# Kernel tuning notes

Hardware: AMD Instinct MI355X
Metric: run time of the kernel (lower is better)

Reference implementation:

```python
import jax, jax.numpy as jnp
import numpy as np

B, C, H, W = 64, 3, 224, 224
PH = PW = 16
GH, GW = H // PH, W // PW
NP = GH * GW                        # 196 patches
E = 512                             # embed_dim == decoder_dim
NH = 8                              # num_heads
PPD = C * PH * PW                   # 768 pixels per patch
MASK_RATIO = 0.75
NUM_MASKED = int(MASK_RATIO * NP)   # 147


def setup_inputs() -> dict:
    key = jax.random.key(0)
    ks = jax.random.split(key, 16)
    s = 0.02
    x = jax.random.normal(ks[0], (B, C, H, W), jnp.float32)
    # per-sample random permutation (torch.rand().argsort() equivalent)
    shuffle_indices = jax.vmap(lambda k: jax.random.permutation(k, NP))(
        jax.random.split(ks[1], B)).astype(jnp.int32)
    return {
        "x": x,
        "shuffle_indices": shuffle_indices,
        "W_pe": jax.random.normal(ks[2], (E, PPD), jnp.float32) * s,
        "b_pe": jnp.zeros((E,), jnp.float32),
        "pos_embed": jax.random.normal(ks[3], (1, NP, E), jnp.float32),
        "enc_W": jax.random.normal(ks[4], (E, E), jnp.float32) * s,
        "enc_b": jnp.zeros((E,), jnp.float32),
        "in_proj_w": jax.random.normal(ks[5], (3 * E, E), jnp.float32) * s,
        "in_proj_b": jnp.zeros((3 * E,), jnp.float32),
        "out_w": jax.random.normal(ks[6], (E, E), jnp.float32) * s,
        "out_b": jnp.zeros((E,), jnp.float32),
        "head_W": jax.random.normal(ks[7], (PPD, E), jnp.float32) * s,
        "head_b": jnp.zeros((PPD,), jnp.float32),
        # torch.randn_like(mask_patches) noise, passed in for determinism
        "noise": jax.random.normal(ks[8], (B, NUM_MASKED, PPD), jnp.float32),
    }


def _to_img(p):
    # [b, nP, ph*pw*c] -> [b, c, H, W] (inverse of patchify)
    return p.reshape(B, GH, GW, PH, PW, C).transpose(0, 5, 1, 3, 2, 4).reshape(B, C, H, W)


def reference(x, shuffle_indices, W_pe, b_pe, pos_embed, enc_W, enc_b,
              in_proj_w, in_proj_b, out_w, out_b, head_W, head_b, noise):
    hd = E // NH
    # patchify: [b,c,H,W] -> [b, nP, ph*pw*c]
    patches = x.reshape(B, C, GH, PH, GW, PW).transpose(0, 2, 4, 3, 5, 1).reshape(B, NP, PPD)

    mask_ind = shuffle_indices[:, :NUM_MASKED]      # [b, 147]
    unmask_ind = shuffle_indices[:, NUM_MASKED:]    # [b, 49]
    bi = jnp.arange(B)[:, None]
    mask_patches = patches[bi, mask_ind]            # [b,147,768]
    unmask_patches = patches[bi, unmask_ind]        # [b, 49,768]

    # mask_image: unmasked patches copied from x, masked patches = 1
    is_masked = jnp.zeros((B, NP), bool).at[bi, mask_ind].set(True)
    mpix = is_masked.reshape(B, 1, GH, 1, GW, 1)
    mpix = jnp.broadcast_to(mpix, (B, C, GH, PH, GW, PW)).reshape(B, C, H, W)
    mask_image = jnp.where(mpix, jnp.ones_like(x), x)

    # encode visible tokens
    pe = pos_embed[0]                               # [nP, E]
    unmask_tokens = unmask_patches @ W_pe.T + b_pe + pe[unmask_ind]
    encoded = jax.nn.gelu(unmask_tokens @ enc_W.T + enc_b)   # encoder.transformer stand-in

    # decode: cross attention (queries = mask tokens, kv = encoded)
    mask_tokens = mask_patches @ W_pe.T + b_pe + pe[mask_ind]
    Wq, Wk, Wv = jnp.split(in_proj_w, 3)
    bq, bk, bv = jnp.split(in_proj_b, 3)
    q = (mask_tokens @ Wq.T + bq).reshape(B, NUM_MASKED, NH, hd)
    k = (encoded @ Wk.T + bk).reshape(B, -1, NH, hd)
    v = (encoded @ Wv.T + bv).reshape(B, -1, NH, hd)
    attn = jax.nn.softmax(jnp.einsum('bqhd,bkhd->bhqk', q, k) / jnp.sqrt(jnp.float32(hd)), axis=-1)
    attn_out = jnp.einsum('bhqk,bkhd->bqhd', attn, v).reshape(B, NUM_MASKED, E) @ out_w.T + out_b

    # scatter encoded + attended tokens back into full sequence
    output_tokens = (jnp.zeros((B, NP, E), x.dtype)
                     .at[bi, unmask_ind].set(encoded)
                     .at[bi, mask_ind].set(attn_out))
    dec_mask_tokens = output_tokens[bi, mask_ind]
    pred = dec_mask_tokens @ head_W.T + head_b      # [b,147,768]

    mse_all_patches = jnp.abs(pred - mask_patches).mean(axis=-1).mean()

    recons_patches = jax.lax.stop_gradient(patches).at[bi, mask_ind].set(pred)
    recons_img = _to_img(recons_patches)

    patches_noisy = patches.at[bi, mask_ind].set(noise)
    patches_to_img = _to_img(patches_noisy)

    return recons_img, patches_to_img, mse_all_patches, mask_image
```

## Files before the change

kernel.cpp:

```cpp
#include <hip/hip_runtime.h>
#include <math.h>

typedef __attribute__((ext_vector_type(8))) __bf16 bf16x8;
typedef __attribute__((ext_vector_type(8))) unsigned short u16x8;
typedef __attribute__((ext_vector_type(4))) unsigned short u16x4;
typedef __attribute__((ext_vector_type(4))) float f32x4;

typedef unsigned int as1_u32 __attribute__((address_space(1)));
typedef unsigned int as3_u32 __attribute__((address_space(3)));

__device__ __forceinline__ float bf2f(unsigned short h){
  return __uint_as_float(((unsigned int)h) << 16);
}
__device__ __forceinline__ unsigned short f2bf(float f){
  unsigned int u = __float_as_uint(f);
  unsigned int r = (u + 0x7FFFu + ((u >> 16) & 1u)) >> 16;
  return (unsigned short)r;
}

#if __has_builtin(__builtin_amdgcn_global_load_lds)
#define HAVE_GLOAD_LDS 1
__device__ __forceinline__ void gload16(const void* g, void* l){
  __builtin_amdgcn_global_load_lds((const as1_u32*)(unsigned long long)g,
                                   (as3_u32*)l, 16, 0, 0);
}
#else
#define HAVE_GLOAD_LDS 0
#endif

__global__ __launch_bounds__(256) void prep_all(
    const int* __restrict__ shuf, int* __restrict__ slot, int* __restrict__ invp,
    const float* __restrict__ Wpe, const float* __restrict__ outw,
    unsigned short* __restrict__ WpeT, unsigned short* __restrict__ outwT,
    const float* __restrict__ encW, const float* __restrict__ inW,
    const float* __restrict__ headW, unsigned short* __restrict__ wcat,
    const float* __restrict__ pos, const float* __restrict__ b_pe,
    const float* __restrict__ outb, const float* __restrict__ headb,
    unsigned short* __restrict__ pe2b, float* __restrict__ bh32)
{
  const int bid = blockIdx.x, t = threadIdx.x;
  __shared__ float tile[32][33];
  if (bid < 49){
    const int i = bid*256 + t;
    if (i < 64*196){
      const int b = i / 196, j = i % 196;
      const int p = shuf[b*196 + j];
      slot[b*196 + p] = (j < 147) ? j : -1;
      invp[b*196 + p] = j;
    }
  } else if (bid < 689){
    int b2 = bid - 49;
    const float* src; unsigned short* dst; int R, C, bx, by;
    if (b2 < 384){ src = Wpe;  dst = WpeT;  R = 512; C = 768; bx = b2 % 24; by = b2 / 24; }
    else { b2 -= 384; src = outw; dst = outwT; R = 512; C = 512; bx = b2 % 16; by = b2 / 16; }
    const int tx = t & 31, ty = t >> 5;
    #pragma unroll
    for (int i = 0; i < 4; i++)
      tile[ty + i*8][tx] = src[(size_t)(by*32 + ty + i*8)*C + bx*32 + tx];
    __syncthreads();
    #pragma unroll
    for (int i = 0; i < 4; i++)
      dst[(size_t)(bx*32 + ty + i*8)*R + by*32 + tx] = f2bf(tile[tx][ty + i*8]);
  } else if (bid < 2097){
    const int i = ((bid - 689)*256 + t) * 4;
    f32x4 v;
    if      (i <  262144) v = *(const f32x4*)(encW + i);
    else if (i < 1048576) v = *(const f32x4*)(inW + (i - 262144));
    else                  v = *(const f32x4*)(headW + (i - 1048576));
    u16x4 o = { f2bf(v[0]), f2bf(v[1]), f2bf(v[2]), f2bf(v[3]) };
    *(u16x4*)(wcat + i) = o;
  } else if (bid < 2225){
    const int i = ((bid - 2097)*256 + t) * 4;
    u16x4 o = {0, 0, 0, 0};
    if (i < 100352){
      const f32x4 pv = *(const f32x4*)(pos + i);
      const f32x4 bv = *(const f32x4*)(b_pe + (i & 511));
      o = u16x4{ f2bf(pv[0]+bv[0]), f2bf(pv[1]+bv[1]), f2bf(pv[2]+bv[2]), f2bf(pv[3]+bv[3]) };
    }
    *(u16x4*)(pe2b + i) = o;
  } else {
    const int r = (bid - 2225)*64 + (t >> 2);
    const int q4 = t & 3;
    float a = 0.0f;
    const float* hw = headW + (size_t)r*512 + q4*128;
    const float* ob = outb + q4*128;
    for (int e = 0; e < 128; e++) a += hw[e] * ob[e];
    a += __shfl_down(a, 2, 4);
    a += __shfl_down(a, 1, 4);
    if (q4 == 0) bh32[r] = a + headb[r];
  }
}

struct GD {
  const unsigned short* A; const unsigned short* W; const float* aux;
  const int* tok; unsigned short* ob; float* of;
  int N, K, mode, blk0, nx;
};

__device__ __forceinline__ void gemm_core(const GD g, int local, unsigned char* smem){
  const int tn = (local % g.nx) * 64;
  const int tm = (local / g.nx) * 128;
  const int N = g.N, K = g.K;
  unsigned short* As = (unsigned short*)smem;
  unsigned short* Bs = (unsigned short*)(smem + 2*128*32*2);
  const int t = threadIdx.x;
  const int wave = t >> 6, lane = t & 63;
  const int wr = (wave >> 1) * 64, wc = (wave & 1) * 32;
  const int lr = lane & 15, lg = lane >> 4;

  f32x4 acc[4][2] = {};
  const int nt = K >> 5;

#if HAVE_GLOAD_LDS
  const int srow = lane >> 2;
  const int scol = (lane & 3) * 8;
  const unsigned short* Ag = g.A + (size_t)(tm + wave*32 + srow) * K + scol;
  const unsigned short* Bg = g.W + (size_t)(tn + wave*16 + srow) * K + scol;
  const size_t rstepA = (size_t)16 * K;

  auto issue = [&](int tile_i, int slot_i){
    const int k0 = tile_i * 32;
    unsigned short* Al = As + slot_i*(128*32) + wave*(32*32);
    unsigned short* Bl = Bs + slot_i*(64*32)  + wave*(16*32);
    gload16(Ag + k0,          Al);
    gload16(Ag + k0 + rstepA, Al + 16*32);
    gload16(Bg + k0,          Bl);
  };

  issue(0, 0);
  __syncthreads();

  for (int tt = 0; tt < nt; ++tt){
    const int cur = tt & 1;
    if (tt + 1 < nt) issue(tt + 1, cur ^ 1);
    const unsigned short* Ab = As + cur*(128*32);
    const unsigned short* Bb = Bs + cur*(64*32);
    bf16x8 av[4], bv[2];
    #pragma unroll
    for (int mi = 0; mi < 4; mi++) av[mi] = *(const bf16x8*)&Ab[(wr + mi*16 + lr)*32 + lg*8];
    #pragma unroll
    for (int ni = 0; ni < 2; ni++) bv[ni] = *(const bf16x8*)&Bb[(wc + ni*16 + lr)*32 + lg*8];
    #pragma unroll
    for (int mi = 0; mi < 4; mi++)
      #pragma unroll
      for (int ni = 0; ni < 2; ni++)
        acc[mi][ni] = __builtin_amdgcn_mfma_f32_16x16x32_bf16(av[mi], bv[ni], acc[mi][ni], 0, 0, 0);
    __syncthreads();
  }
#else
  unsigned short* As1 = (unsigned short*)smem;
  unsigned short* Bs1 = (unsigned short*)(smem + 128*32*2);
  const int r0 = t >> 2;
  const int c0 = (t & 3) * 8;
  for (int k0 = 0; k0 < K; k0 += 32){
    u16x8 ra0 = *(const u16x8*)(g.A + (size_t)(tm + r0) * K + k0 + c0);
    u16x8 rb0 = (r0 < 64) ? *(const u16x8*)(g.W + (size_t)(tn + r0) * K + k0 + c0) : u16x8{};
    __syncthreads();
    *(u16x8*)&As1[r0 * 32 + c0] = ra0;
    if (r0 < 64) *(u16x8*)&Bs1[r0 * 32 + c0] = rb0;
    __syncthreads();
    bf16x8 av[4], bv[2];
    #pragma unroll
    for (int mi = 0; mi < 4; mi++) av[mi] = *(const bf16x8*)&As1[(wr + mi*16 + lr)*32 + lg*8];
    #pragma unroll
    for (int ni = 0; ni < 2; ni++) bv[ni] = *(const bf16x8*)&Bs1[(wc + ni*16 + lr)*32 + lg*8];
    #pragma unroll
    for (int mi = 0; mi < 4; mi++)
      #pragma unroll
      for (int ni = 0; ni < 2; ni++)
        acc[mi][ni] = __builtin_amdgcn_mfma_f32_16x16x32_bf16(av[mi], bv[ni], acc[mi][ni], 0, 0, 0);
  }
#endif

  const int mode = g.mode;
  #pragma unroll
  for (int ni = 0; ni < 2; ni++){
    const int gcol = tn + wc + ni*16 + lr;
    const float bval = (mode == 0 || mode == 3) ? g.aux[gcol] : 0.0f;
    #pragma unroll
    for (int mi = 0; mi < 4; mi++){
      #pragma unroll
      for (int jj = 0; jj < 4; jj++){
        const int grow = tm + wr + mi*16 + lg*4 + jj;
        float v = acc[mi][ni][jj] + bval;
        if (mode == 1 || mode == 2) v += g.aux[(size_t)(g.tok[grow] & 255) * 512 + gcol];
        if (mode == 2){
          const float u = v;
          v = 0.5f * u * (1.0f + tanhf(0.7978845608f * (u + 0.044715f * u * u * u)));
        }
        if (mode == 3) g.of[(size_t)grow * N + gcol] = v;
        else           g.ob[(size_t)grow * N + gcol] = f2bf(v);
      }
    }
  }
}

__global__ __launch_bounds__(256) void gemm_one(GD g){
  __shared__ __align__(16) unsigned char smem[24576];
  gemm_core(g, blockIdx.x, smem);
}
__global__ __launch_bounds__(256) void gemm_two(GD a, GD b){
  __shared__ __align__(16) unsigned char smem[24576];
  GD g = (blockIdx.x >= b.blk0) ? b : a;
  gemm_core(g, blockIdx.x - g.blk0, smem);
}

__global__ __launch_bounds__(256) void fold_patch(GD g0, GD g1, GD g2, GD g3, GD g4,
    const float* __restrict__ x, const int* __restrict__ invp,
    unsigned short* __restrict__ maskA, unsigned short* __restrict__ unmaskA,
    int* __restrict__ tokcat)
{
  __shared__ __align__(16) unsigned char smem[24576];
  const int bid = blockIdx.x, t = threadIdx.x;
  if (bid < 176){
    GD g = g0;
    if (bid >= g1.blk0) g = g1;
    if (bid >= g2.blk0) g = g2;
    if (bid >= g3.blk0) g = g3;
    if (bid >= g4.blk0) g = g4;
    gemm_core(g, bid - g.blk0, smem);
    return;
  }
  const int blk = bid - 176;
  const int b = blk / 14, gh = blk % 14;
  unsigned short* ld = (unsigned short*)smem;
  for (int e = t; e < 2688; e += 256){
    const int w4 = e % 56, rest = e / 56;
    const int phi = rest & 15, c = rest >> 4;
    const f32x4 v4 = *(const f32x4*)(x + (size_t)b*150528 + c*50176
                                     + (size_t)(gh*16 + phi)*224 + w4*4);
    const int gw = w4 >> 2, part = w4 & 3;
    const int dbase = gw*768 + phi*48 + part*12 + c;
    ld[dbase]     = f2bf(v4[0]);
    ld[dbase + 3] = f2bf(v4[1]);
    ld[dbase + 6] = f2bf(v4[2]);
    ld[dbase + 9] = f2bf(v4[3]);
  }
  __syncthreads();
  for (int e = t; e < 1344; e += 256){
    const int gw = e / 96, elem8 = e % 96;
    const int p = gh*14 + gw;
    const int j = invp[b*196 + p];
    unsigned short* dst;
    int row;
    if (j < 147){ row = b*160 + j;        dst = maskA; }
    else        { row = b*64 + (j - 147); dst = unmaskA; }
    *(u16x8*)&dst[(size_t)row*768 + elem8*8] = *(const u16x8*)&ld[gw*768 + elem8*8];
    if (elem8 == 0) tokcat[(j < 147) ? (b*160 + j) : (10240 + b*64 + (j - 147))] = p;
  }
}

__global__ __launch_bounds__(256) void attn_mfma(const unsigned short* __restrict__ qb,
                                                 const unsigned short* __restrict__ kv,
                                                 unsigned short* __restrict__ attnout)
{
  __shared__ __align__(16) unsigned char smem[72064];
  unsigned short* qs  = (unsigned short*)smem;
  unsigned short* ks  = (unsigned short*)(smem + 27648);
  unsigned short* vsT = (unsigned short*)(smem + 36864);
  unsigned short* pwt = (unsigned short*)(smem + 46080);
  float* inv_ = (float*)(smem + 71424);
  const int b = blockIdx.x >> 3, h = blockIdx.x & 7;
  const int t = threadIdx.x;
  const int wave = t >> 6, lane = t & 63;
  const int wr = (wave >> 1) * 96, wc = (wave & 1) * 32;
  const int lr = lane & 15, lg = lane >> 4;

  for (int idx = t; idx < 192*8; idx += 256){
    const int i = idx >> 3, g = idx & 7;
    u16x8 v = {};
    if (i < 160) v = *(const u16x8*)(qb + (size_t)(b*160 + i)*512 + h*64 + g*8);
    *(u16x8*)&qs[i*72 + g*8] = v;
  }
  for (int idx = t; idx < 64*8; idx += 256){
    const int j = idx >> 3, g = idx & 7;
    const size_t base = (size_t)(b*64 + j)*1024 + h*64 + g*8;
    u16x8 k8 = *(const u16x8*)(kv + base);
    u16x8 v8 = *(const u16x8*)(kv + base + 512);
    *(u16x8*)&ks[j*72 + g*8] = k8;
    #pragma unroll
    for (int d = 0; d < 8; d++) vsT[(g*8 + d)*72 + j] = v8[d];
  }
  __syncthreads();

  {
    f32x4 acc[6][2] = {};
    #pragma unroll
    for (int ksv = 0; ksv < 2; ksv++){
      const int kk = ksv*32;
      bf16x8 av[6], bv[2];
      #pragma unroll
      for (int mi = 0; mi < 6; mi++) av[mi] = *(const bf16x8*)&qs[(wr + mi*16 + lr)*72 + kk + lg*8];
      #pragma unroll
      for (int ni = 0; ni < 2; ni++) bv[ni] = *(const bf16x8*)&ks[(wc + ni*16 + lr)*72 + kk + lg*8];
      #pragma unroll
      for (int mi = 0; mi < 6; mi++)
        #pragma unroll
        for (int ni = 0; ni < 2; ni++)
          acc[mi][ni] = __builtin_amdgcn_mfma_f32_16x16x32_bf16(av[mi], bv[ni], acc[mi][ni], 0, 0, 0);
    }
    #pragma unroll
    for (int mi = 0; mi < 6; mi++)
      #pragma unroll
      for (int ni = 0; ni < 2; ni++)
        #pragma unroll
        for (int jj = 0; jj < 4; jj++)
          pwt[(wr + mi*16 + lg*4 + jj)*66 + wc + ni*16 + lr] = f2bf(acc[mi][ni][jj] * 0.125f);
  }
  __syncthreads();

  unsigned short* pa = qs;
  if (t < 147){
    float sc[49];
    float m = -1e30f;
    #pragma unroll 7
    for (int j = 0; j < 49; j++){ sc[j] = bf2f(pwt[t*66 + j]); m = fmaxf(m, sc[j]); }
    float sum = 0.0f;
    for (int j = 0; j < 49; j++){
      const float e = __expf(sc[j] - m);
      sum += e;
      pa[t*72 + j] = f2bf(e);
    }
    inv_[t] = 1.0f / sum;
    for (int j = 49; j < 64; j++) pa[t*72 + j] = 0;
  } else if (t < 192){
    for (int j = 0; j < 64; j++) pa[t*72 + j] = 0;
    if (t < 160) inv_[t] = 0.0f;
  }
  __syncthreads();

  {
    f32x4 acc[6][2] = {};
    #pragma unroll
    for (int ksv = 0; ksv < 2; ksv++){
      const int kk = ksv*32;
      bf16x8 av[6], bv[2];
      #pragma unroll
      for (int mi = 0; mi < 6; mi++) av[mi] = *(const bf16x8*)&pa[(wr + mi*16 + lr)*72 + kk + lg*8];
      #pragma unroll
      for (int ni = 0; ni < 2; ni++) bv[ni] = *(const bf16x8*)&vsT[(wc + ni*16 + lr)*72 + kk + lg*8];
      #pragma unroll
      for (int mi = 0; mi < 6; mi++)
        #pragma unroll
        for (int ni = 0; ni < 2; ni++)
          acc[mi][ni] = __builtin_amdgcn_mfma_f32_16x16x32_bf16(av[mi], bv[ni], acc[mi][ni], 0, 0, 0);
    }
    #pragma unroll
    for (int mi = 0; mi < 6; mi++)
      #pragma unroll
      for (int ni = 0; ni < 2; ni++)
        #pragma unroll
        for (int jj = 0; jj < 4; jj++){
          const int grow = wr + mi*16 + lg*4 + jj;
          if (grow < 160){
            const float v = acc[mi][ni][jj] * inv_[grow];
            attnout[(size_t)(b*160 + grow)*512 + h*64 + wc + ni*16 + lr] = f2bf(v);
          }
        }
  }
}

__global__ __launch_bounds__(256) void finalize_k(const float* __restrict__ x, const int* __restrict__ slot,
                           const unsigned short* __restrict__ predb, const float* __restrict__ noise,
                           float* __restrict__ out, float* __restrict__ partial)
{
  const int i4 = blockIdx.x * 256 + threadIdx.x;
  const int idx = i4 * 4;
  const int w = idx % 224;
  const int h = (idx / 224) % 224;
  const int c = (idx / 50176) % 3;
  const int b = idx / 150528;
  const f32x4 xv = *(const f32x4*)(x + idx);
  const int p = (h >> 4) * 14 + (w >> 4);
  const int s = slot[b*196 + p];
  f32x4 rec = xv, noi = xv, mim = xv;
  float a = 0.0f;
  if (s >= 0){
    const int d = (h & 15)*48 + (w & 15)*3 + c;
    const size_t pb = (size_t)(b*160 + s)*768 + d;
    const size_t nb = (size_t)(b*147 + s)*768 + d;
    rec = f32x4{bf2f(predb[pb]), bf2f(predb[pb+3]), bf2f(predb[pb+6]), bf2f(predb[pb+9])};
    noi = f32x4{noise[nb], noise[nb+3], noise[nb+6], noise[nb+9]};
    mim = f32x4{1.0f, 1.0f, 1.0f, 1.0f};
    a = fabsf(rec[0] - xv[0]) + fabsf(rec[1] - xv[1]) + fabsf(rec[2] - xv[2]) + fabsf(rec[3] - xv[3]);
  }
  *(f32x4*)(out + idx) = rec;
  *(f32x4*)(out + 9633792 + idx) = noi;
  float prevm = __shfl_up(mim[3], 1);
  if ((threadIdx.x & 63) == 0 && idx > 0){
    const int pidx = idx - 1;
    const int pw2 = pidx % 224, ph2 = (pidx / 224) % 224;
    const int pb2 = pidx / 150528;
    const int pp = (ph2 >> 4) * 14 + (pw2 >> 4);
    prevm = (slot[pb2*196 + pp] >= 0) ? 1.0f : x[pidx];
  }
  *(f32x4*)(out + 19267584 + idx) = f32x4{prevm, mim[0], mim[1], mim[2]};
  if (i4 == 2408447) out[28901376] = mim[3];
  #pragma unroll
  for (int o = 32; o > 0; o >>= 1) a += __shfl_down(a, o);
  __shared__ float wsum[4];
  if ((threadIdx.x & 63) == 0) wsum[threadIdx.x >> 6] = a;
  __syncthreads();
  if (threadIdx.x == 0)
    partial[blockIdx.x] = wsum[0] + wsum[1] + wsum[2] + wsum[3];
}

__global__ __launch_bounds__(1024) void mse_reduce(const float* __restrict__ partial, float* __restrict__ out){
  float a = 0.0f;
  for (int i = threadIdx.x; i < 9408; i += 1024) a += partial[i];
  #pragma unroll
  for (int o = 32; o > 0; o >>= 1) a += __shfl_down(a, o);
  __shared__ float wsum[16];
  if ((threadIdx.x & 63) == 0) wsum[threadIdx.x >> 6] = a;
  __syncthreads();
  if (threadIdx.x == 0){
    float s = 0.0f;
    #pragma unroll
    for (int i = 0; i < 16; i++) s += wsum[i];
    out[19267584] = s * (1.0f / 7225344.0f);
  }
}

extern "C" void kernel_launch(void* const* d_in, const int* in_sizes, int n_in,
                              void* d_out, int out_size, void* d_ws, size_t ws_size,
                              hipStream_t stream)
{
  const float* x     = (const float*)d_in[0];
  const int*   shuf  = (const int*)d_in[1];
  const float* W_pe  = (const float*)d_in[2];
  const float* b_pe  = (const float*)d_in[3];
  const float* pos   = (const float*)d_in[4];
  const float* encW  = (const float*)d_in[5];
  const float* encB  = (const float*)d_in[6];
  const float* inW   = (const float*)d_in[7];
  const float* inB   = (const float*)d_in[8];
  const float* outW  = (const float*)d_in[9];
  const float* outB  = (const float*)d_in[10];
  const float* headW = (const float*)d_in[11];
  const float* headB = (const float*)d_in[12];
  const float* noise = (const float*)d_in[13];
  float* out = (float*)d_out;

  char* ws = (char*)d_ws;
  size_t cur = 0;
  auto alloc = [&](size_t bytes){ size_t o = cur; cur += (bytes + 255) & ~(size_t)255; return o; };

  int*   slot    = (int*)(ws + alloc(64*196*4));
  int*   invp    = (int*)(ws + alloc(64*196*4));
  int*   tokcat  = (int*)(ws + alloc(14336*4));
  float* partial = (float*)(ws + alloc(9408*4));
  unsigned short* wcat    = (unsigned short*)(ws + alloc((size_t)1441792*2));
  unsigned short* encw_b  = wcat;
  unsigned short* inw_b   = wcat +  262144;
  unsigned short* headw_b = wcat + 1048576;
  unsigned short* WpeT  = (unsigned short*)(ws + alloc((size_t)393216*2));
  unsigned short* outwT = (unsigned short*)(ws + alloc((size_t)262144*2));
  unsigned short* Wqpe  = (unsigned short*)(ws + alloc((size_t)393216*2));
  unsigned short* Wepe  = (unsigned short*)(ws + alloc((size_t)393216*2));
  unsigned short* Whp   = (unsigned short*)(ws + alloc((size_t)393216*2));
  unsigned short* pe2b  = (unsigned short*)(ws + alloc((size_t)131072*2));
  float* peq  = (float*)(ws + alloc((size_t)131072*4));
  float* pee  = (float*)(ws + alloc((size_t)131072*4));
  float* bh32 = (float*)(ws + alloc(768*4));
  unsigned short* maskA   = (unsigned short*)(ws + alloc((size_t)7864320*2));
  unsigned short* unmaskA = (unsigned short*)(ws + alloc((size_t)3145728*2));
  unsigned short* attnout = (unsigned short*)(ws + alloc((size_t)5242880*2));
  unsigned short* predb   = (unsigned short*)(ws + alloc((size_t)7864320*2));
  unsigned short* enc   = (unsigned short*)(ws + alloc((size_t)2097152*2));
  unsigned short* qb    = (unsigned short*)(ws + alloc((size_t)5242880*2));
  unsigned short* kvb   = (unsigned short*)(ws + alloc((size_t)4194304*2));

  prep_all<<<2237, 256, 0, stream>>>(shuf, slot, invp, W_pe, outW, WpeT, outwT,
                                     encW, inW, headW, wcat,
                                     pos, b_pe, outB, headB, pe2b, bh32);

  {
    GD t1 = { inw_b,  WpeT,   nullptr, nullptr, Wqpe,   nullptr, 768, 512, 4,   0, 12 };
    GD t2 = { encw_b, WpeT,   nullptr, nullptr, Wepe,   nullptr, 768, 512, 4,  48, 12 };
    GD t3 = { headw_b,outwT,  nullptr, nullptr, Whp,    nullptr, 512, 512, 4,  96,  8 };
    GD t4 = { pe2b,   inw_b,  inB,     nullptr, nullptr, peq,    512, 512, 3, 144,  8 };
    GD t5 = { pe2b,   encw_b, encB,    nullptr, nullptr, pee,    512, 512, 3, 160,  8 };
    fold_patch<<<1072, 256, 0, stream>>>(t1, t2, t3, t4, t5, x, invp, maskA, unmaskA, tokcat);
  }
  {
    GD q  = { maskA,   Wqpe, peq, tokcat,         qb,  nullptr, 512, 768, 1,   0, 8 };
    GD en = { unmaskA, Wepe, pee, tokcat + 10240, enc, nullptr, 512, 768, 2, 640, 8 };
    gemm_two<<<896, 256, 0, stream>>>(q, en);
  }
  {
    GD kv = { enc, inw_b + (size_t)512*512, inB + 512, nullptr, kvb, nullptr, 1024, 512, 0, 0, 16 };
    gemm_one<<<512, 256, 0, stream>>>(kv);
  }
  attn_mfma<<<512, 256, 0, stream>>>(qb, kvb, attnout);
  {
    GD pr = { attnout, Whp, bh32, nullptr, predb, nullptr, 768, 512, 0, 0, 12 };
    gemm_one<<<960, 256, 0, stream>>>(pr);
  }

  finalize_k<<<9408, 256, 0, stream>>>(x, slot, predb, noise, out, partial);
  mse_reduce<<<1, 1024, 0, stream>>>(partial, out);
}
```

Baseline: 180.5 us.

## Stage masked patch predictions and noise in LDS per patch row in finalize

The finalize kernel now assigns one block per (batch, patch-row). It cooperatively loads the masked patches' bf16 predictions and fp32 noise into shared memory with vectorized coalesced reads, replacing the old strided scalar gathers from global memory. The per-pixel output writes then read from LDS, and the partial sum count shrinks so the final reduction is a single pass. The block grid drops to 896 blocks of 512 threads, which may reduce parallelism and adds about 64KB of LDS per block, lowering occupancy. Boundary handling for the shifted mask output is adjusted for row starts.

```diff
diff --git a/kernel.cpp b/kernel.cpp
--- a/kernel.cpp
+++ b/kernel.cpp
@@ -360,63 +360,88 @@
   }
 }
 
-__global__ __launch_bounds__(256) void finalize_k(const float* __restrict__ x, const int* __restrict__ slot,
+__global__ __launch_bounds__(512) void finalize_k(const float* __restrict__ x, const int* __restrict__ slot,
                            const unsigned short* __restrict__ predb, const float* __restrict__ noise,
                            float* __restrict__ out, float* __restrict__ partial)
 {
-  const int i4 = blockIdx.x * 256 + threadIdx.x;
-  const int idx = i4 * 4;
-  const int w = idx % 224;
-  const int h = (idx / 224) % 224;
-  const int c = (idx / 50176) % 3;
-  const int b = idx / 150528;
-  const f32x4 xv = *(const f32x4*)(x + idx);
-  const int p = (h >> 4) * 14 + (w >> 4);
-  const int s = slot[b*196 + p];
-  f32x4 rec = xv, noi = xv, mim = xv;
+  __shared__ int slot_s[14];
+  __shared__ unsigned short pred_s[14*768];
+  __shared__ float noi_s[14*768];
+  __shared__ float wsum[8];
+  const int blk = blockIdx.x;
+  const int b = blk / 14, gh = blk % 14;
+  const int t = threadIdx.x;
+
+  if (t < 14) slot_s[t] = slot[b*196 + gh*14 + t];
+  __syncthreads();
+  for (int e = t; e < 14*96; e += 512){
+    const int gw = e / 96, k = e % 96;
+    const int s = slot_s[gw];
+    if (s >= 0)
+      *(u16x8*)&pred_s[gw*768 + k*8] = *(const u16x8*)(predb + (size_t)(b*160 + s)*768 + k*8);
+  }
+  for (int e = t; e < 14*192; e += 512){
+    const int gw = e / 192, k = e % 192;
+    const int s = slot_s[gw];
+    if (s >= 0)
+      *(f32x4*)&noi_s[gw*768 + k*4] = *(const f32x4*)(noise + (size_t)(b*147 + s)*768 + k*4);
+  }
+  __syncthreads();
+
   float a = 0.0f;
-  if (s >= 0){
-    const int d = (h & 15)*48 + (w & 15)*3 + c;
-    const size_t pb = (size_t)(b*160 + s)*768 + d;
-    const size_t nb = (size_t)(b*147 + s)*768 + d;
-    rec = f32x4{bf2f(predb[pb]), bf2f(predb[pb+3]), bf2f(predb[pb+6]), bf2f(predb[pb+9])};
-    noi = f32x4{noise[nb], noise[nb+3], noise[nb+6], noise[nb+9]};
-    mim = f32x4{1.0f, 1.0f, 1.0f, 1.0f};
-    a = fabsf(rec[0] - xv[0]) + fabsf(rec[1] - xv[1]) + fabsf(rec[2] - xv[2]) + fabsf(rec[3] - xv[3]);
-  }
-  *(f32x4*)(out + idx) = rec;
-  *(f32x4*)(out + 9633792 + idx) = noi;
-  float prevm = __shfl_up(mim[3], 1);
-  if ((threadIdx.x & 63) == 0 && idx > 0){
-    const int pidx = idx - 1;
-    const int pw2 = pidx % 224, ph2 = (pidx / 224) % 224;
-    const int pb2 = pidx / 150528;
-    const int pp = (ph2 >> 4) * 14 + (pw2 >> 4);
-    prevm = (slot[pb2*196 + pp] >= 0) ? 1.0f : x[pidx];
-  }
-  *(f32x4*)(out + 19267584 + idx) = f32x4{prevm, mim[0], mim[1], mim[2]};
-  if (i4 == 2408447) out[28901376] = mim[3];
+  for (int e = t; e < 2688; e += 512){
+    const int w4 = e % 56, rest = e / 56;
+    const int phi = rest & 15, c = rest >> 4;
+    const int gw = w4 >> 2, part = w4 & 3;
+    const int idx = b*150528 + c*50176 + (gh*16 + phi)*224 + w4*4;
+    const f32x4 xv = *(const f32x4*)(x + idx);
+    const int s = slot_s[gw];
+    f32x4 rec = xv, noi = xv, mim = xv;
+    if (s >= 0){
+      const int dbase = gw*768 + phi*48 + part*12 + c;
+      rec = f32x4{bf2f(pred_s[dbase]), bf2f(pred_s[dbase+3]), bf2f(pred_s[dbase+6]), bf2f(pred_s[dbase+9])};
+      noi = f32x4{noi_s[dbase], noi_s[dbase+3], noi_s[dbase+6], noi_s[dbase+9]};
+      mim = f32x4{1.0f, 1.0f, 1.0f, 1.0f};
+      a += fabsf(rec[0]-xv[0]) + fabsf(rec[1]-xv[1]) + fabsf(rec[2]-xv[2]) + fabsf(rec[3]-xv[3]);
+    }
+    *(f32x4*)(out + idx) = rec;
+    *(f32x4*)(out + 9633792 + idx) = noi;
+    float prevm = __shfl_up(mim[3], 1);
+    if ((t & 63) == 0 || w4 == 0){
+      const int pidx = idx - 1;
+      if (pidx >= 0){
+        const int w2 = pidx % 224, h2 = (pidx / 224) % 224;
+        const int b2 = pidx / 150528;
+        const int p2i = (h2 >> 4) * 14 + (w2 >> 4);
+        prevm = (slot[b2*196 + p2i] >= 0) ? 1.0f : x[pidx];
+      } else prevm = 0.0f;
+    }
+    *(f32x4*)(out + 19267584 + idx) = f32x4{prevm, mim[0], mim[1], mim[2]};
+    if (idx == 9633788) out[28901376] = mim[3];
+  }
   #pragma unroll
   for (int o = 32; o > 0; o >>= 1) a += __shfl_down(a, o);
-  __shared__ float wsum[4];
-  if ((threadIdx.x & 63) == 0) wsum[threadIdx.x >> 6] = a;
-  __syncthreads();
-  if (threadIdx.x == 0)
-    partial[blockIdx.x] = wsum[0] + wsum[1] + wsum[2] + wsum[3];
-}
-
-__global__ __launch_bounds__(1024) void mse_reduce(const float* __restrict__ partial, float* __restrict__ out){
-  float a = 0.0f;
-  for (int i = threadIdx.x; i < 9408; i += 1024) a += partial[i];
+  if ((t & 63) == 0) wsum[t >> 6] = a;
+  __syncthreads();
+  if (t == 0){
+    float s8 = 0.0f;
+    #pragma unroll
+    for (int i = 0; i < 8; i++) s8 += wsum[i];
+    partial[blk] = s8;
+  }
+}
+
+__global__ __launch_bounds__(896) void mse_reduce(const float* __restrict__ partial, float* __restrict__ out){
+  float a = (threadIdx.x < 896) ? partial[threadIdx.x] : 0.0f;
   #pragma unroll
   for (int o = 32; o > 0; o >>= 1) a += __shfl_down(a, o);
-  __shared__ float wsum[16];
+  __shared__ float wsum[14];
   if ((threadIdx.x & 63) == 0) wsum[threadIdx.x >> 6] = a;
   __syncthreads();
   if (threadIdx.x == 0){
     float s = 0.0f;
     #pragma unroll
-    for (int i = 0; i < 16; i++) s += wsum[i];
+    for (int i = 0; i < 14; i++) s += wsum[i];
     out[19267584] = s * (1.0f / 7225344.0f);
   }
 }
@@ -448,7 +473,7 @@
   int*   slot    = (int*)(ws + alloc(64*196*4));
   int*   invp    = (int*)(ws + alloc(64*196*4));
   int*   tokcat  = (int*)(ws + alloc(14336*4));
-  float* partial = (float*)(ws + alloc(9408*4));
+  float* partial = (float*)(ws + alloc(896*4));
   unsigned short* wcat    = (unsigned short*)(ws + alloc((size_t)1441792*2));
   unsigned short* encw_b  = wcat;
   unsigned short* inw_b   = wcat +  262144;
@@ -497,6 +522,6 @@
     gemm_one<<<960, 256, 0, stream>>>(pr);
   }
 
-  finalize_k<<<9408, 256, 0, stream>>>(x, slot, predb, noise, out, partial);
-  mse_reduce<<<1, 1024, 0, stream>>>(partial, out);
-}
+  finalize_k<<<896, 512, 0, stream>>>(x, slot, predb, noise, out, partial);
+  mse_reduce<<<1, 896, 0, stream>>>(partial, out);
+}
```

Result: faster. 170.2 us, median of 2 (-5.7%).
